# Kernel optimization log

Hardware: AMD Instinct MI355X
Metric: run time of the kernel (lower is better)

The kernel has to match this reference:

```python
import jax, jax.numpy as jnp
import numpy as np

NUM_RBF = 16
MAX_REL = 32          # max_relative_feature
AUTOREGRESSIVE = True
D_MIN, D_MAX = 2.0, 22.0
LN_EPS = 1e-5


def setup_inputs() -> dict:
    key = jax.random.key(0)
    ks = jax.random.split(key, 6)
    B, L, A, K = 1, 1280, 14, 30
    E_feat, edge_in = 128, 16 + NUM_RBF * 4 * 10  # 656
    X = jax.random.normal(ks[0], (B, L, A, 3), dtype=jnp.float32) * 3.0
    residue_idx = jnp.tile(jnp.arange(L, dtype=jnp.int32)[None], (B, 1))
    chain_labels = jnp.zeros((B, L), dtype=jnp.int32)
    E_idx = jax.random.randint(ks[1], (B, L, K), 0, L, dtype=jnp.int32)
    atom_mask = jnp.ones((B, L, A), dtype=jnp.float32)
    W_pos = jax.random.normal(ks[2], (2 * MAX_REL + 2, 16), dtype=jnp.float32) * 0.1
    b_pos = jnp.zeros((16,), dtype=jnp.float32)
    W_edge = jax.random.normal(ks[3], (edge_in, E_feat), dtype=jnp.float32) * 0.05
    ln_gamma = jnp.ones((E_feat,), dtype=jnp.float32)
    ln_beta = jnp.zeros((E_feat,), dtype=jnp.float32)
    return {"X": X, "residue_idx": residue_idx, "chain_labels": chain_labels,
            "E_idx": E_idx, "atom_mask": atom_mask, "W_pos": W_pos,
            "b_pos": b_pos, "W_edge": W_edge, "ln_gamma": ln_gamma,
            "ln_beta": ln_beta}


def _forward(X, residue_idx, chain_labels, E_idx, W_pos, b_pos, W_edge,
             ln_gamma, ln_beta):
    B, L, A, _ = X.shape
    K = E_idx.shape[-1]
    # backbone atoms in loop order [Ca, N, C, O] -> X indices [1, 0, 2, 3]
    bb = X[:, :, jnp.array([1, 0, 2, 3]), :]          # [B, L, 4, 3]
    sc = X[:, :, 4:, :]                               # [B, L, 10, 3]
    Abb = jnp.transpose(bb, (0, 2, 1, 3))             # [B, 4, L, 3]
    Asc = jnp.transpose(sc, (0, 2, 1, 3))             # [B, 10, L, 3]
    # dense pairwise distances for all 40 (bb, sc) atom pairs: [B,4,10,L,L]
    diff = Abb[:, :, None, :, None, :] - Asc[:, None, :, None, :, :]
    D = jnp.sqrt(jnp.sum(diff * diff, axis=-1) + 1e-6)
    # gather top-k neighbor columns -> [B,4,10,L,K]
    D_nb = jnp.take_along_axis(D, E_idx[:, None, None, :, :], axis=4)
    mu = jnp.linspace(D_MIN, D_MAX, NUM_RBF, dtype=D_nb.dtype)
    sigma = (D_MAX - D_MIN) / NUM_RBF
    RBF = jnp.exp(-(((D_nb[..., None] - mu) / sigma) ** 2))  # [B,4,10,L,K,16]
    if AUTOREGRESSIVE:
        self_edges = (E_idx == jnp.arange(L, dtype=E_idx.dtype)[None, :, None])
        RBF = jnp.where(self_edges[:, None, None, :, :, None], 0.0, RBF)
    # concat order: bb outer, sc inner -> [B,L,K, 4*10*16]
    RBF_all = jnp.transpose(RBF, (0, 3, 4, 1, 2, 5)).reshape(B, L, K, 4 * 10 * NUM_RBF)
    # positional encodings
    offset = residue_idx[:, :, None] - residue_idx[:, None, :]        # [B,L,L]
    offset = jnp.take_along_axis(offset, E_idx, axis=2)               # [B,L,K]
    d_chains = (chain_labels[:, :, None] == chain_labels[:, None, :]).astype(jnp.int32)
    E_chains = jnp.take_along_axis(d_chains, E_idx, axis=2)           # [B,L,K]
    d = jnp.clip(offset + MAX_REL, 0, 2 * MAX_REL) * E_chains + (1 - E_chains) * (2 * MAX_REL + 1)
    d_onehot = jax.nn.one_hot(d, 2 * MAX_REL + 2, dtype=W_pos.dtype)  # [B,L,K,66]
    E_positional = d_onehot @ W_pos + b_pos                           # [B,L,K,16]
    E = jnp.concatenate([E_positional, RBF_all], axis=-1)             # [B,L,K,656]
    E = E @ W_edge                                                    # no bias
    # LayerNorm over last dim
    mean = jnp.mean(E, axis=-1, keepdims=True)
    var = jnp.mean((E - mean) ** 2, axis=-1, keepdims=True)
    E = (E - mean) / jnp.sqrt(var + LN_EPS) * ln_gamma + ln_beta
    return E


def reference(X, residue_idx, chain_labels, E_idx, atom_mask, W_pos, b_pos,
              W_edge, ln_gamma, ln_beta):
    E = _forward(X, residue_idx, chain_labels, E_idx, W_pos, b_pos, W_edge,
                 ln_gamma, ln_beta)
    return (E, E_idx)
```

## Files before the change

kernel.cpp:

```cpp
#include <hip/hip_runtime.h>

typedef short bf16x8 __attribute__((ext_vector_type(8)));
typedef float f32x4  __attribute__((ext_vector_type(4)));

#define L_RES 1280
#define A_ATM 14
#define K_NB  30
#define EPB   15
#define FEAT  656
#define KPAD  672
#define NCH   128
#define AF_STRIDE 680
#define E_OUT_OFF (L_RES * K_NB * NCH)

__device__ __forceinline__ ushort f2bf(float x) {
    union { float f; unsigned u; } v; v.f = x;
    unsigned r = (v.u + 0x7fffu + ((v.u >> 16) & 1u)) >> 16;
    return (ushort)r;
}

__global__ __launch_bounds__(256) void wt_convert_kernel(const float* __restrict__ W,
                                                         ushort* __restrict__ Wt) {
    int idx = blockIdx.x * 256 + threadIdx.x;
    if (idx >= NCH * KPAD) return;
    int n = idx / KPAD, k = idx - n * KPAD;
    float v = (k < FEAT) ? W[k * NCH + n] : 0.0f;
    Wt[idx] = f2bf(v);
}

__global__ __launch_bounds__(256, 7) void sidechain_feat_kernel(
    const float* __restrict__ X,
    const int*   __restrict__ ridx,
    const int*   __restrict__ clab,
    const int*   __restrict__ Eidx,
    const float* __restrict__ Wpos,
    const float* __restrict__ bpos,
    const ushort* __restrict__ Wt,
    const float* __restrict__ gamma,
    const float* __restrict__ beta,
    float* __restrict__ out)
{
    __shared__ __align__(16) ushort Af[16][AF_STRIDE];
    __shared__ __align__(16) float part[16][4][2];

    const int blk  = blockIdx.x;
    const int i    = blk >> 1;
    const int h    = blk & 1;
    const int ebase = h * EPB;
    const int t    = threadIdx.x;
    const int w    = t >> 6;
    const int lane = t & 63;
    const int frow = lane & 15;
    const int quad = lane >> 4;
    const int c0 = w * 32 + frow;
    const int c1 = c0 + 16;

    const ushort* B0p = Wt + (size_t)c0 * KPAD + quad * 8;
    const ushort* B1p = Wt + (size_t)c1 * KPAD + quad * 8;
    bf16x8 b0c = *(const bf16x8*)(B0p);
    bf16x8 b1c = *(const bf16x8*)(B1p);
    bf16x8 b0n = *(const bf16x8*)(B0p + 32);
    bf16x8 b1n = *(const bf16x8*)(B1p + 32);
    float gg0 = gamma[c0], gg1 = gamma[c1];
    float be0 = beta[c0],  be1 = beta[c1];

    if (t < EPB)
        out[E_OUT_OFF + i * K_NB + ebase + t] = (float)Eidx[i * K_NB + ebase + t];

    const int my_clab = clab[i];
    const int my_ridx = ridx[i];

    if (t < EPB * 16) {
        int e = t >> 4, c = t & 15;
        int j = Eidx[i * K_NB + ebase + e];
        int d;
        if (my_clab == clab[j]) {
            int off = my_ridx - ridx[j] + 32;
            d = off < 0 ? 0 : (off > 64 ? 64 : off);
        } else {
            d = 65;
        }
        Af[e][c] = f2bf(Wpos[d * 16 + c] + bpos[c]);
    }
    if (t < EPB * 16) Af[t >> 4][FEAT + (t & 15)] = 0;

#pragma unroll
    for (int u = 0; u < 3; ++u) {
        int idx = t + u * 256;
        if (idx < EPB * 40) {
            int e  = idx / 40;
            int p  = idx - e * 40;
            int ab = p / 10, as = p - ab * 10;
            const int perm[4] = {1, 0, 2, 3};
            int j = Eidx[i * K_NB + ebase + e];
            const float* xb = X + (size_t)(i * A_ATM + perm[ab]) * 3;
            const float* xp = X + (size_t)(j * A_ATM + 4 + as) * 3;
            float dx = xb[0] - xp[0];
            float dy = xb[1] - xp[1];
            float dz = xb[2] - xp[2];
            float dist = sqrtf(dx * dx + dy * dy + dz * dz + 1e-6f);
            bool self = (j == i);
            unsigned* dst = (unsigned*)&Af[e][16 + p * 16];
#pragma unroll
            for (int q = 0; q < 8; ++q) {
                float m0 = 2.0f + (float)(2 * q)     * (20.0f / 15.0f);
                float m1 = 2.0f + (float)(2 * q + 1) * (20.0f / 15.0f);
                float a0 = (dist - m0) * 0.8f;
                float a1 = (dist - m1) * 0.8f;
                float r0 = self ? 0.0f : __expf(-a0 * a0);
                float r1 = self ? 0.0f : __expf(-a1 * a1);
                unsigned pk;
                asm("v_cvt_pk_bf16_f32 %0, %1, %2" : "=v"(pk) : "v"(r0), "v"(r1));
                dst[q] = pk;
            }
        }
    }
    __syncthreads();

    const ushort* A0p = &Af[frow][quad * 8];
    bf16x8 a0c = *(const bf16x8*)(A0p);

    f32x4 acc00 = {0.f,0.f,0.f,0.f}, acc01 = {0.f,0.f,0.f,0.f};

#pragma unroll
    for (int c = 0; c < 21; ++c) {
        bf16x8 ua0 = a0c, ub0 = b0c, ub1 = b1c;
        if (c + 1 < 21)
            a0c = *(const bf16x8*)(A0p + (c + 1) * 32);
        b0c = b0n; b1c = b1n;
        if (c + 2 < 21) {
            b0n = *(const bf16x8*)(B0p + (c + 2) * 32);
            b1n = *(const bf16x8*)(B1p + (c + 2) * 32);
        }
        acc00 = __builtin_amdgcn_mfma_f32_16x16x32_bf16(ua0, ub0, acc00, 0, 0, 0);
        acc01 = __builtin_amdgcn_mfma_f32_16x16x32_bf16(ua0, ub1, acc01, 0, 0, 0);
    }

    float s0[4], q0[4];
#pragma unroll
    for (int r = 0; r < 4; ++r) {
        s0[r] = acc00[r] + acc01[r];
        q0[r] = acc00[r] * acc00[r] + acc01[r] * acc01[r];
    }
#pragma unroll
    for (int off = 1; off < 16; off <<= 1) {
#pragma unroll
        for (int r = 0; r < 4; ++r) {
            s0[r] += __shfl_xor(s0[r], off);
            q0[r] += __shfl_xor(q0[r], off);
        }
    }
    if (frow == 0) {
#pragma unroll
        for (int r = 0; r < 4; ++r) {
            int row = quad * 4 + r;
            part[row][w][0] = s0[r];
            part[row][w][1] = q0[r];
        }
    }
    __syncthreads();

#pragma unroll
    for (int r = 0; r < 4; ++r) {
        int row = quad * 4 + r;
        if (row < EPB) {
            f32x4 pa = *(const f32x4*)&part[row][0][0];
            f32x4 pb = *(const f32x4*)&part[row][2][0];
            float S = pa[0] + pa[2] + pb[0] + pb[2];
            float Q = pa[1] + pa[3] + pb[1] + pb[3];
            float mean = S * (1.0f / 128.0f);
            float rstd = rsqrtf(Q * (1.0f / 128.0f) - mean * mean + 1e-5f);
            float* o = out + (size_t)(i * K_NB + ebase + row) * NCH;
            o[c0] = (acc00[r] - mean) * rstd * gg0 + be0;
            o[c1] = (acc01[r] - mean) * rstd * gg1 + be1;
        }
    }
}

extern "C" void kernel_launch(void* const* d_in, const int* in_sizes, int n_in,
                              void* d_out, int out_size, void* d_ws, size_t ws_size,
                              hipStream_t stream) {
    const float* X     = (const float*)d_in[0];
    const int*   ridx  = (const int*)  d_in[1];
    const int*   clab  = (const int*)  d_in[2];
    const int*   Eidx  = (const int*)  d_in[3];
    const float* Wpos  = (const float*)d_in[5];
    const float* bpos  = (const float*)d_in[6];
    const float* Wedge = (const float*)d_in[7];
    const float* gamma = (const float*)d_in[8];
    const float* beta  = (const float*)d_in[9];
    float* out = (float*)d_out;

    ushort* Wt = (ushort*)d_ws;

    wt_convert_kernel<<<(NCH * KPAD + 255) / 256, 256, 0, stream>>>(Wedge, Wt);
    sidechain_feat_kernel<<<2 * L_RES, 256, 0, stream>>>(
        X, ridx, clab, Eidx, Wpos, bpos, Wt, gamma, beta, out);
}
```

Measured before the change: 109.9 us.

## Process all 30 neighbors per block with 8 waves sharing weight tiles

```diff
diff --git a/kernel.cpp b/kernel.cpp
--- a/kernel.cpp
+++ b/kernel.cpp
@@ -6,10 +6,10 @@
 #define L_RES 1280
 #define A_ATM 14
 #define K_NB  30
-#define EPB   15
 #define FEAT  656
 #define KPAD  672
 #define NCH   128
+#define WAVES 8
 #define AF_STRIDE 680
 #define E_OUT_OFF (L_RES * K_NB * NCH)
 
@@ -28,7 +28,7 @@
     Wt[idx] = f2bf(v);
 }
 
-__global__ __launch_bounds__(256, 7) void sidechain_feat_kernel(
+__global__ __launch_bounds__(512, 6) void sidechain_feat_kernel(
     const float* __restrict__ X,
     const int*   __restrict__ ridx,
     const int*   __restrict__ clab,
@@ -40,39 +40,26 @@
     const float* __restrict__ beta,
     float* __restrict__ out)
 {
-    __shared__ __align__(16) ushort Af[16][AF_STRIDE];
-    __shared__ __align__(16) float part[16][4][2];
-
-    const int blk  = blockIdx.x;
-    const int i    = blk >> 1;
-    const int h    = blk & 1;
-    const int ebase = h * EPB;
+    __shared__ __align__(16) ushort Af[32][AF_STRIDE];
+    __shared__ __align__(16) float part[32][WAVES][2];
+
+    const int i    = blockIdx.x;
     const int t    = threadIdx.x;
     const int w    = t >> 6;
     const int lane = t & 63;
     const int frow = lane & 15;
     const int quad = lane >> 4;
-    const int c0 = w * 32 + frow;
-    const int c1 = c0 + 16;
-
-    const ushort* B0p = Wt + (size_t)c0 * KPAD + quad * 8;
-    const ushort* B1p = Wt + (size_t)c1 * KPAD + quad * 8;
-    bf16x8 b0c = *(const bf16x8*)(B0p);
-    bf16x8 b1c = *(const bf16x8*)(B1p);
-    bf16x8 b0n = *(const bf16x8*)(B0p + 32);
-    bf16x8 b1n = *(const bf16x8*)(B1p + 32);
-    float gg0 = gamma[c0], gg1 = gamma[c1];
-    float be0 = beta[c0],  be1 = beta[c1];
-
-    if (t < EPB)
-        out[E_OUT_OFF + i * K_NB + ebase + t] = (float)Eidx[i * K_NB + ebase + t];
+    const int c0   = w * 16 + frow;
+
+    if (t < K_NB)
+        out[E_OUT_OFF + i * K_NB + t] = (float)Eidx[i * K_NB + t];
 
     const int my_clab = clab[i];
     const int my_ridx = ridx[i];
 
-    if (t < EPB * 16) {
+    if (t < K_NB * 16) {
         int e = t >> 4, c = t & 15;
-        int j = Eidx[i * K_NB + ebase + e];
+        int j = Eidx[i * K_NB + e];
         int d;
         if (my_clab == clab[j]) {
             int off = my_ridx - ridx[j] + 32;
@@ -82,17 +69,23 @@
         }
         Af[e][c] = f2bf(Wpos[d * 16 + c] + bpos[c]);
     }
-    if (t < EPB * 16) Af[t >> 4][FEAT + (t & 15)] = 0;
+    if (t < K_NB * 16) Af[t >> 4][FEAT + (t & 15)] = 0;
+
+    const ushort* B0p = Wt + (size_t)c0 * KPAD + quad * 8;
+    bf16x8 b0 = *(const bf16x8*)(B0p);
+    bf16x8 b1 = *(const bf16x8*)(B0p + 32);
+    bf16x8 b2 = *(const bf16x8*)(B0p + 64);
+    float gg = gamma[c0], be = beta[c0];
 
 #pragma unroll
     for (int u = 0; u < 3; ++u) {
-        int idx = t + u * 256;
-        if (idx < EPB * 40) {
+        int idx = t + u * 512;
+        if (idx < K_NB * 40) {
             int e  = idx / 40;
             int p  = idx - e * 40;
             int ab = p / 10, as = p - ab * 10;
             const int perm[4] = {1, 0, 2, 3};
-            int j = Eidx[i * K_NB + ebase + e];
+            int j = Eidx[i * K_NB + e];
             const float* xb = X + (size_t)(i * A_ATM + perm[ab]) * 3;
             const float* xp = X + (size_t)(j * A_ATM + 4 + as) * 3;
             float dx = xb[0] - xp[0];
@@ -118,29 +111,33 @@
     __syncthreads();
 
     const ushort* A0p = &Af[frow][quad * 8];
-    bf16x8 a0c = *(const bf16x8*)(A0p);
-
-    f32x4 acc00 = {0.f,0.f,0.f,0.f}, acc01 = {0.f,0.f,0.f,0.f};
+    const ushort* A1p = &Af[16 + frow][quad * 8];
+    bf16x8 a0 = *(const bf16x8*)(A0p);
+    bf16x8 a1 = *(const bf16x8*)(A1p);
+
+    f32x4 acc0 = {0.f,0.f,0.f,0.f}, acc1 = {0.f,0.f,0.f,0.f};
 
 #pragma unroll
     for (int c = 0; c < 21; ++c) {
-        bf16x8 ua0 = a0c, ub0 = b0c, ub1 = b1c;
-        if (c + 1 < 21)
-            a0c = *(const bf16x8*)(A0p + (c + 1) * 32);
-        b0c = b0n; b1c = b1n;
-        if (c + 2 < 21) {
-            b0n = *(const bf16x8*)(B0p + (c + 2) * 32);
-            b1n = *(const bf16x8*)(B1p + (c + 2) * 32);
-        }
-        acc00 = __builtin_amdgcn_mfma_f32_16x16x32_bf16(ua0, ub0, acc00, 0, 0, 0);
-        acc01 = __builtin_amdgcn_mfma_f32_16x16x32_bf16(ua0, ub1, acc01, 0, 0, 0);
-    }
-
-    float s0[4], q0[4];
+        bf16x8 ua0 = a0, ua1 = a1, ub = b0;
+        if (c + 1 < 21) {
+            a0 = *(const bf16x8*)(A0p + (c + 1) * 32);
+            a1 = *(const bf16x8*)(A1p + (c + 1) * 32);
+        }
+        b0 = b1; b1 = b2;
+        if (c + 3 < 21)
+            b2 = *(const bf16x8*)(B0p + (c + 3) * 32);
+        acc0 = __builtin_amdgcn_mfma_f32_16x16x32_bf16(ua0, ub, acc0, 0, 0, 0);
+        acc1 = __builtin_amdgcn_mfma_f32_16x16x32_bf16(ua1, ub, acc1, 0, 0, 0);
+    }
+
+    float s0[4], q0[4], s1[4], q1[4];
 #pragma unroll
     for (int r = 0; r < 4; ++r) {
-        s0[r] = acc00[r] + acc01[r];
-        q0[r] = acc00[r] * acc00[r] + acc01[r] * acc01[r];
+        s0[r] = acc0[r];
+        q0[r] = acc0[r] * acc0[r];
+        s1[r] = acc1[r];
+        q1[r] = acc1[r] * acc1[r];
     }
 #pragma unroll
     for (int off = 1; off < 16; off <<= 1) {
@@ -148,14 +145,18 @@
         for (int r = 0; r < 4; ++r) {
             s0[r] += __shfl_xor(s0[r], off);
             q0[r] += __shfl_xor(q0[r], off);
+            s1[r] += __shfl_xor(s1[r], off);
+            q1[r] += __shfl_xor(q1[r], off);
         }
     }
     if (frow == 0) {
 #pragma unroll
         for (int r = 0; r < 4; ++r) {
             int row = quad * 4 + r;
-            part[row][w][0] = s0[r];
-            part[row][w][1] = q0[r];
+            part[row][w][0]      = s0[r];
+            part[row][w][1]      = q0[r];
+            part[16 + row][w][0] = s1[r];
+            part[16 + row][w][1] = q1[r];
         }
     }
     __syncthreads();
@@ -163,16 +164,28 @@
 #pragma unroll
     for (int r = 0; r < 4; ++r) {
         int row = quad * 4 + r;
-        if (row < EPB) {
+        {
             f32x4 pa = *(const f32x4*)&part[row][0][0];
             f32x4 pb = *(const f32x4*)&part[row][2][0];
-            float S = pa[0] + pa[2] + pb[0] + pb[2];
-            float Q = pa[1] + pa[3] + pb[1] + pb[3];
+            f32x4 pc = *(const f32x4*)&part[row][4][0];
+            f32x4 pd = *(const f32x4*)&part[row][6][0];
+            float S = pa[0] + pa[2] + pb[0] + pb[2] + pc[0] + pc[2] + pd[0] + pd[2];
+            float Q = pa[1] + pa[3] + pb[1] + pb[3] + pc[1] + pc[3] + pd[1] + pd[3];
             float mean = S * (1.0f / 128.0f);
             float rstd = rsqrtf(Q * (1.0f / 128.0f) - mean * mean + 1e-5f);
-            float* o = out + (size_t)(i * K_NB + ebase + row) * NCH;
-            o[c0] = (acc00[r] - mean) * rstd * gg0 + be0;
-            o[c1] = (acc01[r] - mean) * rstd * gg1 + be1;
+            out[(size_t)(i * K_NB + row) * NCH + c0] = (acc0[r] - mean) * rstd * gg + be;
+        }
+        int row1 = 16 + row;
+        if (row1 < K_NB) {
+            f32x4 pa = *(const f32x4*)&part[row1][0][0];
+            f32x4 pb = *(const f32x4*)&part[row1][2][0];
+            f32x4 pc = *(const f32x4*)&part[row1][4][0];
+            f32x4 pd = *(const f32x4*)&part[row1][6][0];
+            float S = pa[0] + pa[2] + pb[0] + pb[2] + pc[0] + pc[2] + pd[0] + pd[2];
+            float Q = pa[1] + pa[3] + pb[1] + pb[3] + pc[1] + pc[3] + pd[1] + pd[3];
+            float mean = S * (1.0f / 128.0f);
+            float rstd = rsqrtf(Q * (1.0f / 128.0f) - mean * mean + 1e-5f);
+            out[(size_t)(i * K_NB + row1) * NCH + c0] = (acc1[r] - mean) * rstd * gg + be;
         }
     }
 }
@@ -194,6 +207,6 @@
     ushort* Wt = (ushort*)d_ws;
 
     wt_convert_kernel<<<(NCH * KPAD + 255) / 256, 256, 0, stream>>>(Wedge, Wt);
-    sidechain_feat_kernel<<<2 * L_RES, 256, 0, stream>>>(
+    sidechain_feat_kernel<<<L_RES, 512, 0, stream>>>(
         X, ridx, clab, Eidx, Wpos, bpos, Wt, gamma, beta, out);
 }
```

Measured after the change: 105.1 us. -4.4%, faster.
